# Performance work log

Measured on AMD Instinct MI355X. Metric: run time of the kernel, lower is better.

Reference implementation:

```python
import jax, jax.numpy as jnp
import numpy as np

B, S, D_MODEL, D_K, D_V = 4, 2048, 1024, 1024, 1024


def setup_inputs() -> dict:
    key = jax.random.key(0)
    k1, k2, k3, k4 = jax.random.split(key, 4)
    scale = 1.0 / np.sqrt(D_MODEL)
    x = jax.random.normal(k1, (B, S, D_MODEL), dtype=jnp.float32)
    Wq = jax.random.normal(k2, (D_K, D_MODEL), dtype=jnp.float32) * scale
    Wk = jax.random.normal(k3, (D_K, D_MODEL), dtype=jnp.float32) * scale
    Wv = jax.random.normal(k4, (D_V, D_MODEL), dtype=jnp.float32) * scale
    # causal mask: position i may attend to j <= i (True = keep)
    mask = jnp.broadcast_to(jnp.tril(jnp.ones((S, S), dtype=bool)), (B, S, S))
    return {"x": x, "mask": mask, "Wq": Wq, "Wk": Wk, "Wv": Wv}


def reference(x, mask, Wq, Wk, Wv):
    # nn.Linear(d, k, bias=False): y = x @ W.T with W of shape [k, d]
    q = jnp.einsum('bsd,kd->bsk', x, Wq)
    k = jnp.einsum('bsd,kd->bsk', x, Wk)
    v = jnp.einsum('bsd,vd->bsv', x, Wv)
    scores = jnp.einsum('bik,bjk->bij', q, k) / jnp.sqrt(jnp.float32(D_K))
    s = jnp.where(mask, scores, -jnp.inf)
    # masked, fully-masked-row-safe softmax (fully masked rows -> all zeros,
    # matching softmax[all-masked rows] = 0 in the original)
    m = jnp.max(s, axis=-1, keepdims=True)
    m_safe = jnp.where(jnp.isfinite(m), m, 0.0)
    e = jnp.exp(s - m_safe)          # exp(-inf) = 0 for masked entries
    denom = jnp.sum(e, axis=-1, keepdims=True)
    p = e / jnp.where(denom == 0.0, 1.0, denom)
    return jnp.einsum('bij,bjv->biv', p, v)
```

## Files before the change

### kernel.cpp

```cpp
#include <hip/hip_runtime.h>
#include <hip/hip_bf16.h>
#include <stdint.h>

#define SEQ   2048
#define DM    1024
#define NBAT  4

typedef __attribute__((ext_vector_type(8))) short  short8;
typedef __attribute__((ext_vector_type(4))) float  floatx4;

__device__ __forceinline__ unsigned short f2b(float f) {
    __hip_bfloat16 h = __float2bfloat16(f);
    unsigned short r;
    __builtin_memcpy(&r, &h, 2);
    return r;
}

__device__ __forceinline__ void gload16(const void* g, void* s) {
    __builtin_amdgcn_global_load_lds(
        (const __attribute__((address_space(1))) unsigned int*)(uintptr_t)g,
        (__attribute__((address_space(3))) unsigned int*)(uintptr_t)s,
        16, 0, 0);
}

__global__ void cast_bf16_4(const float4* __restrict__ in, ushort4* __restrict__ out, int n4) {
    int i = blockIdx.x * 256 + threadIdx.x;
    if (i < n4) {
        float4 f = in[i];
        ushort4 u;
        u.x = f2b(f.x); u.y = f2b(f.y); u.z = f2b(f.z); u.w = f2b(f.w);
        out[i] = u;
    }
}

__global__ void zero_f32(float* __restrict__ p, int n) {
    int i = blockIdx.x * 256 + threadIdx.x;
    if (i < n) p[i] = 0.f;
}

template<int OUTM, bool TRI, bool KLIM, bool REV>
__global__ __launch_bounds__(256) void gemm_bt(
    const unsigned short* __restrict__ A, const unsigned short* __restrict__ Bm,
    void* __restrict__ Cv,
    unsigned short* __restrict__ Qo, unsigned short* __restrict__ Ko,
    unsigned short* __restrict__ Vto,
    float* __restrict__ rowsum,
    int M, int N, int K,
    long long sA, long long sB, long long sC, float qscale)
{
    int m0, n0;
    if (TRI) {
        const int f = blockIdx.x;
        int ti = (int)((sqrtf(8.f * f + 1.f) - 1.f) * 0.5f);
        if ((ti + 1) * (ti + 2) / 2 <= f) ti++;
        if (ti * (ti + 1) / 2 > f) ti--;
        const int tj = f - ti * (ti + 1) / 2;
        m0 = ti * 128;
        n0 = tj * 128;
    } else {
        m0 = (REV ? (gridDim.y - 1 - blockIdx.y) : blockIdx.y) * 128;
        n0 = blockIdx.x * 128;
    }
    const int z = blockIdx.z;
    A  += (size_t)z * sA;
    Bm += (size_t)z * sB;

    __shared__ __align__(16) unsigned short As[128 * 32];
    __shared__ __align__(16) unsigned short Bs[128 * 32];

    const int t    = threadIdx.x;
    const int w    = t >> 6;
    const int lane = t & 63;
    const int wr   = w >> 1, wc = w & 1;
    const int r    = lane & 15, q = lane >> 4;

    floatx4 acc[4][4];
#pragma unroll
    for (int i = 0; i < 4; i++)
#pragma unroll
        for (int j = 0; j < 4; j++)
            acc[i][j] = (floatx4){0.f, 0.f, 0.f, 0.f};

    const int kEnd = KLIM ? ((m0 + 128 < K) ? m0 + 128 : K) : K;

    const int row0 = t >> 2;
    const int cc0  = t & 3;

    for (int k0 = 0; k0 < kEnd; k0 += 32) {
        const size_t ka = (size_t)k0 + cc0 * 8;
        gload16(A  + (size_t)(m0 + row0)      * K + ka, As + (size_t)w * 512);
        gload16(A  + (size_t)(m0 + row0 + 64) * K + ka, As + 2048 + (size_t)w * 512);
        gload16(Bm + (size_t)(n0 + row0)      * K + ka, Bs + (size_t)w * 512);
        gload16(Bm + (size_t)(n0 + row0 + 64) * K + ka, Bs + 2048 + (size_t)w * 512);
        __builtin_amdgcn_s_waitcnt(0);
        __syncthreads();

        short8 af[4], bf[4];
#pragma unroll
        for (int i = 0; i < 4; i++) {
            af[i] = *(const short8*)&As[(wr * 64 + i * 16 + r) * 32 + q * 8];
            bf[i] = *(const short8*)&Bs[(wc * 64 + i * 16 + r) * 32 + q * 8];
        }
#pragma unroll
        for (int i = 0; i < 4; i++)
#pragma unroll
            for (int j = 0; j < 4; j++)
                acc[i][j] = __builtin_amdgcn_mfma_f32_16x16x32_bf16(af[i], bf[j], acc[i][j], 0, 0, 0);
        __syncthreads();
    }

    const int gmb = m0 + wr * 64 + q * 4;
    const int gnb = n0 + wc * 64 + r;
    if (OUTM == 3) {
#pragma unroll
        for (int i = 0; i < 4; i++) {
            const int gm = gmb + i * 16;
#pragma unroll
            for (int j = 0; j < 4; j++) {
                const int gn = gnb + j * 16;
                if (n0 < 1024) {
#pragma unroll
                    for (int rr = 0; rr < 4; rr++)
                        Qo[(size_t)(gm + rr) * 1024 + gn] = f2b(acc[i][j][rr] * qscale);
                } else if (n0 < 2048) {
#pragma unroll
                    for (int rr = 0; rr < 4; rr++)
                        Ko[(size_t)(gm + rr) * 1024 + (gn - 1024)] = f2b(acc[i][j][rr]);
                } else {
                    const int b = gm >> 11;
                    const int s = gm & 2047;
                    const int v = gn - 2048;
                    ushort4 u;
                    u.x = f2b(acc[i][j][0]);
                    u.y = f2b(acc[i][j][1]);
                    u.z = f2b(acc[i][j][2]);
                    u.w = f2b(acc[i][j][3]);
                    *(ushort4*)&Vto[((size_t)(b * 1024 + v)) * 2048 + s] = u;
                }
            }
        }
    } else if (OUTM == 4) {
        unsigned short* E = (unsigned short*)Cv + (size_t)z * sC;
        float* rs = rowsum + (size_t)z * SEQ;
#pragma unroll
        for (int i = 0; i < 4; i++) {
            const int gm = gmb + i * 16;
#pragma unroll
            for (int rr = 0; rr < 4; rr++) {
                float part = 0.f;
#pragma unroll
                for (int j = 0; j < 4; j++) {
                    const int gn = gnb + j * 16;
                    const float ev = (gn <= gm + rr) ? __expf(acc[i][j][rr]) : 0.f;
                    part += ev;
                    E[(size_t)(gm + rr) * N + gn] = f2b(ev);
                }
#pragma unroll
                for (int off = 1; off <= 8; off <<= 1)
                    part += __shfl_xor(part, off, 64);
                if (r == 0) atomicAdd(&rs[gm + rr], part);
            }
        }
    } else {
        float* C = (float*)Cv + (size_t)z * sC;
        const float* rs = rowsum + (size_t)z * SEQ;
#pragma unroll
        for (int i = 0; i < 4; i++) {
            const int gm = gmb + i * 16;
#pragma unroll
            for (int rr = 0; rr < 4; rr++) {
                const float inv = 1.0f / rs[gm + rr];
#pragma unroll
                for (int j = 0; j < 4; j++) {
                    const int gn = gnb + j * 16;
                    C[(size_t)(gm + rr) * N + gn] = acc[i][j][rr] * inv;
                }
            }
        }
    }
}

extern "C" void kernel_launch(void* const* d_in, const int* in_sizes, int n_in,
                              void* d_out, int out_size, void* d_ws, size_t ws_size,
                              hipStream_t stream) {
    (void)in_sizes; (void)n_in; (void)out_size; (void)ws_size;
    const float* x  = (const float*)d_in[0];
    const float* Wq = (const float*)d_in[2];
    const float* Wk = (const float*)d_in[3];
    const float* Wv = (const float*)d_in[4];

    char* base = (char*)d_ws;
    size_t off = 0;
    auto alloc = [&](size_t n) { char* p = base + off; off += (n + 255) & ~(size_t)255; return p; };

    unsigned short* xb   = (unsigned short*)alloc((size_t)NBAT * SEQ * DM * 2);
    unsigned short* wall = (unsigned short*)alloc((size_t)3 * DM * DM * 2);
    unsigned short* Qb   = (unsigned short*)alloc((size_t)NBAT * SEQ * DM * 2);
    unsigned short* Kb   = (unsigned short*)alloc((size_t)NBAT * SEQ * DM * 2);
    unsigned short* Vtb  = (unsigned short*)alloc((size_t)NBAT * DM * SEQ * 2);
    unsigned short* E    = (unsigned short*)alloc((size_t)NBAT * SEQ * SEQ * 2);
    float*          rsum = (float*)alloc((size_t)NBAT * SEQ * 4);

    const dim3 blk(256);

    {
        int n4 = NBAT * SEQ * DM / 4;
        cast_bf16_4<<<dim3((n4 + 255) / 256), blk, 0, stream>>>((const float4*)x, (ushort4*)xb, n4);
        int w4 = DM * DM / 4;
        dim3 wg((w4 + 255) / 256);
        cast_bf16_4<<<wg, blk, 0, stream>>>((const float4*)Wq, (ushort4*)(wall),               w4);
        cast_bf16_4<<<wg, blk, 0, stream>>>((const float4*)Wk, (ushort4*)(wall + DM * DM),     w4);
        cast_bf16_4<<<wg, blk, 0, stream>>>((const float4*)Wv, (ushort4*)(wall + 2 * DM * DM), w4);
        zero_f32<<<dim3((NBAT * SEQ + 255) / 256), blk, 0, stream>>>(rsum, NBAT * SEQ);
    }

    const int Mtot = NBAT * SEQ;

    gemm_bt<3, false, false, false><<<dim3(3 * DM / 128, Mtot / 128, 1), blk, 0, stream>>>(
        xb, wall, nullptr, Qb, Kb, Vtb, nullptr, Mtot, 3 * DM, DM, 0, 0, 0, 0.03125f);

    gemm_bt<4, true, false, false><<<dim3(136, 1, NBAT), blk, 0, stream>>>(
        Qb, Kb, E, nullptr, nullptr, nullptr, rsum, SEQ, SEQ, DM,
        (long long)SEQ * DM, (long long)SEQ * DM, (long long)SEQ * SEQ, 1.0f);

    gemm_bt<5, false, true, true><<<dim3(DM / 128, SEQ / 128, NBAT), blk, 0, stream>>>(
        E, Vtb, d_out, nullptr, nullptr, nullptr, rsum, SEQ, DM, SEQ,
        (long long)SEQ * SEQ, (long long)DM * SEQ, (long long)SEQ * DM, 1.0f);
}
```

Measured before the change: 308.5 us.

## Fuse score and PV GEMMs into one kernel with per-row-block ready flags

Merges the causal score GEMM and the P·V GEMM into one launch. The row-block ordering is chosen so the larger blocks come first, and each PV tile spin-waits on an atomic counter until every score tile of its row block has written E and the row sums. It also folds the three weight casts into one launch, and the zeroing kernel now clears the counters too. The aim is to remove a launch boundary and the tail idle time between the two attention stages. In exchange it adds spin-waiting, which could deadlock or stall if dependent blocks are scheduled ahead of the blocks they wait on.

```diff
diff --git a/kernel.cpp b/kernel.cpp
--- a/kernel.cpp
+++ b/kernel.cpp
@@ -33,37 +33,31 @@
     }
 }
 
-__global__ void zero_f32(float* __restrict__ p, int n) {
+__global__ void cast_w3(const float4* __restrict__ w0, const float4* __restrict__ w1,
+                        const float4* __restrict__ w2, ushort4* __restrict__ out, int n4) {
+    const float4* srcs[3] = {w0, w1, w2};
     int i = blockIdx.x * 256 + threadIdx.x;
-    if (i < n) p[i] = 0.f;
-}
-
-template<int OUTM, bool TRI, bool KLIM, bool REV>
-__global__ __launch_bounds__(256) void gemm_bt(
+    if (i < n4) {
+        float4 f = srcs[blockIdx.y][i];
+        ushort4 u;
+        u.x = f2b(f.x); u.y = f2b(f.y); u.z = f2b(f.z); u.w = f2b(f.w);
+        out[(size_t)blockIdx.y * n4 + i] = u;
+    }
+}
+
+__global__ void zero_u32(unsigned int* __restrict__ p, int n) {
+    int i = blockIdx.x * 256 + threadIdx.x;
+    if (i < n) p[i] = 0u;
+}
+
+__global__ __launch_bounds__(256) void qkv_gemm(
     const unsigned short* __restrict__ A, const unsigned short* __restrict__ Bm,
-    void* __restrict__ Cv,
     unsigned short* __restrict__ Qo, unsigned short* __restrict__ Ko,
-    unsigned short* __restrict__ Vto,
-    float* __restrict__ rowsum,
-    int M, int N, int K,
-    long long sA, long long sB, long long sC, float qscale)
+    unsigned short* __restrict__ Vto, float qscale)
 {
-    int m0, n0;
-    if (TRI) {
-        const int f = blockIdx.x;
-        int ti = (int)((sqrtf(8.f * f + 1.f) - 1.f) * 0.5f);
-        if ((ti + 1) * (ti + 2) / 2 <= f) ti++;
-        if (ti * (ti + 1) / 2 > f) ti--;
-        const int tj = f - ti * (ti + 1) / 2;
-        m0 = ti * 128;
-        n0 = tj * 128;
-    } else {
-        m0 = (REV ? (gridDim.y - 1 - blockIdx.y) : blockIdx.y) * 128;
-        n0 = blockIdx.x * 128;
-    }
-    const int z = blockIdx.z;
-    A  += (size_t)z * sA;
-    Bm += (size_t)z * sB;
+    const int m0 = blockIdx.y * 128;
+    const int n0 = blockIdx.x * 128;
+    const int K  = DM;
 
     __shared__ __align__(16) unsigned short As[128 * 32];
     __shared__ __align__(16) unsigned short Bs[128 * 32];
@@ -81,12 +75,10 @@
         for (int j = 0; j < 4; j++)
             acc[i][j] = (floatx4){0.f, 0.f, 0.f, 0.f};
 
-    const int kEnd = KLIM ? ((m0 + 128 < K) ? m0 + 128 : K) : K;
-
     const int row0 = t >> 2;
     const int cc0  = t & 3;
 
-    for (int k0 = 0; k0 < kEnd; k0 += 32) {
+    for (int k0 = 0; k0 < K; k0 += 32) {
         const size_t ka = (size_t)k0 + cc0 * 8;
         gload16(A  + (size_t)(m0 + row0)      * K + ka, As + (size_t)w * 512);
         gload16(A  + (size_t)(m0 + row0 + 64) * K + ka, As + 2048 + (size_t)w * 512);
@@ -111,36 +103,116 @@
 
     const int gmb = m0 + wr * 64 + q * 4;
     const int gnb = n0 + wc * 64 + r;
-    if (OUTM == 3) {
+#pragma unroll
+    for (int i = 0; i < 4; i++) {
+        const int gm = gmb + i * 16;
+#pragma unroll
+        for (int j = 0; j < 4; j++) {
+            const int gn = gnb + j * 16;
+            if (n0 < 1024) {
+#pragma unroll
+                for (int rr = 0; rr < 4; rr++)
+                    Qo[(size_t)(gm + rr) * 1024 + gn] = f2b(acc[i][j][rr] * qscale);
+            } else if (n0 < 2048) {
+#pragma unroll
+                for (int rr = 0; rr < 4; rr++)
+                    Ko[(size_t)(gm + rr) * 1024 + (gn - 1024)] = f2b(acc[i][j][rr]);
+            } else {
+                const int b = gm >> 11;
+                const int s = gm & 2047;
+                const int v = gn - 2048;
+                ushort4 u;
+                u.x = f2b(acc[i][j][0]);
+                u.y = f2b(acc[i][j][1]);
+                u.z = f2b(acc[i][j][2]);
+                u.w = f2b(acc[i][j][3]);
+                *(ushort4*)&Vto[((size_t)(b * 1024 + v)) * 2048 + s] = u;
+            }
+        }
+    }
+}
+
+__global__ __launch_bounds__(256, 5) void attn_fused(
+    const unsigned short* __restrict__ Qb, const unsigned short* __restrict__ Kb,
+    unsigned short* __restrict__ E, const unsigned short* __restrict__ Vtb,
+    float* __restrict__ Out, float* __restrict__ rowsum, int* __restrict__ done)
+{
+    const int z = blockIdx.z;
+    const int g = blockIdx.x;
+    int u = (int)(24.5f - sqrtf(600.25f - 2.0f * (float)g));
+    while (24 * (u + 1) - (u + 1) * u / 2 <= g) u++;
+    while (24 * u - u * (u - 1) / 2 > g) u--;
+    const int ti    = 15 - u;
+    const int local = g - (24 * u - u * (u - 1) / 2);
+    const bool isScore = (local <= ti);
+    const int m0 = ti * 128;
+
+    int n0, lda, ldb, kEnd;
+    const unsigned short *A, *Bm;
+    if (isScore) {
+        n0  = local * 128;
+        A   = Qb + (size_t)z * SEQ * DM;  lda = DM;
+        Bm  = Kb + (size_t)z * SEQ * DM;  ldb = DM;
+        kEnd = DM;
+    } else {
+        n0  = (local - ti - 1) * 128;
+        A   = E   + (size_t)z * SEQ * SEQ; lda = SEQ;
+        Bm  = Vtb + (size_t)z * DM * SEQ;  ldb = SEQ;
+        kEnd = m0 + 128;
+        if (threadIdx.x == 0) {
+            while (__hip_atomic_load(&done[z * 16 + ti], __ATOMIC_ACQUIRE,
+                                     __HIP_MEMORY_SCOPE_AGENT) < ti + 1)
+                __builtin_amdgcn_s_sleep(1);
+        }
+        __syncthreads();
+    }
+
+    __shared__ __align__(16) unsigned short As[128 * 32];
+    __shared__ __align__(16) unsigned short Bs[128 * 32];
+
+    const int t    = threadIdx.x;
+    const int w    = t >> 6;
+    const int lane = t & 63;
+    const int wr   = w >> 1, wc = w & 1;
+    const int r    = lane & 15, q = lane >> 4;
+
+    floatx4 acc[4][4];
+#pragma unroll
+    for (int i = 0; i < 4; i++)
+#pragma unroll
+        for (int j = 0; j < 4; j++)
+            acc[i][j] = (floatx4){0.f, 0.f, 0.f, 0.f};
+
+    const int row0 = t >> 2;
+    const int cc0  = t & 3;
+
+    for (int k0 = 0; k0 < kEnd; k0 += 32) {
+        const size_t ka = (size_t)k0 + cc0 * 8;
+        gload16(A  + (size_t)(m0 + row0)      * lda + ka, As + (size_t)w * 512);
+        gload16(A  + (size_t)(m0 + row0 + 64) * lda + ka, As + 2048 + (size_t)w * 512);
+        gload16(Bm + (size_t)(n0 + row0)      * ldb + ka, Bs + (size_t)w * 512);
+        gload16(Bm + (size_t)(n0 + row0 + 64) * ldb + ka, Bs + 2048 + (size_t)w * 512);
+        __builtin_amdgcn_s_waitcnt(0);
+        __syncthreads();
+
+        short8 af[4], bf[4];
 #pragma unroll
         for (int i = 0; i < 4; i++) {
-            const int gm = gmb + i * 16;
-#pragma unroll
-            for (int j = 0; j < 4; j++) {
-                const int gn = gnb + j * 16;
-                if (n0 < 1024) {
-#pragma unroll
-                    for (int rr = 0; rr < 4; rr++)
-                        Qo[(size_t)(gm + rr) * 1024 + gn] = f2b(acc[i][j][rr] * qscale);
-                } else if (n0 < 2048) {
-#pragma unroll
-                    for (int rr = 0; rr < 4; rr++)
-                        Ko[(size_t)(gm + rr) * 1024 + (gn - 1024)] = f2b(acc[i][j][rr]);
-                } else {
-                    const int b = gm >> 11;
-                    const int s = gm & 2047;
-                    const int v = gn - 2048;
-                    ushort4 u;
-                    u.x = f2b(acc[i][j][0]);
-                    u.y = f2b(acc[i][j][1]);
-                    u.z = f2b(acc[i][j][2]);
-                    u.w = f2b(acc[i][j][3]);
-                    *(ushort4*)&Vto[((size_t)(b * 1024 + v)) * 2048 + s] = u;
-                }
-            }
-        }
-    } else if (OUTM == 4) {
-        unsigned short* E = (unsigned short*)Cv + (size_t)z * sC;
+            af[i] = *(const short8*)&As[(wr * 64 + i * 16 + r) * 32 + q * 8];
+            bf[i] = *(const short8*)&Bs[(wc * 64 + i * 16 + r) * 32 + q * 8];
+        }
+#pragma unroll
+        for (int i = 0; i < 4; i++)
+#pragma unroll
+            for (int j = 0; j < 4; j++)
+                acc[i][j] = __builtin_amdgcn_mfma_f32_16x16x32_bf16(af[i], bf[j], acc[i][j], 0, 0, 0);
+        __syncthreads();
+    }
+
+    const int gmb = m0 + wr * 64 + q * 4;
+    const int gnb = n0 + wc * 64 + r;
+    if (isScore) {
+        unsigned short* Ez = E + (size_t)z * SEQ * SEQ;
         float* rs = rowsum + (size_t)z * SEQ;
 #pragma unroll
         for (int i = 0; i < 4; i++) {
@@ -153,7 +225,7 @@
                     const int gn = gnb + j * 16;
                     const float ev = (gn <= gm + rr) ? __expf(acc[i][j][rr]) : 0.f;
                     part += ev;
-                    E[(size_t)(gm + rr) * N + gn] = f2b(ev);
+                    Ez[(size_t)(gm + rr) * SEQ + gn] = f2b(ev);
                 }
 #pragma unroll
                 for (int off = 1; off <= 8; off <<= 1)
@@ -161,8 +233,13 @@
                 if (r == 0) atomicAdd(&rs[gm + rr], part);
             }
         }
+        __syncthreads();
+        if (t == 0) {
+            __threadfence();
+            atomicAdd(&done[z * 16 + ti], 1);
+        }
     } else {
-        float* C = (float*)Cv + (size_t)z * sC;
+        float* C = Out + (size_t)z * SEQ * DM;
         const float* rs = rowsum + (size_t)z * SEQ;
 #pragma unroll
         for (int i = 0; i < 4; i++) {
@@ -173,7 +250,7 @@
 #pragma unroll
                 for (int j = 0; j < 4; j++) {
                     const int gn = gnb + j * 16;
-                    C[(size_t)(gm + rr) * N + gn] = acc[i][j][rr] * inv;
+                    C[(size_t)(gm + rr) * DM + gn] = acc[i][j][rr] * inv;
                 }
             }
         }
@@ -199,7 +276,8 @@
     unsigned short* Kb   = (unsigned short*)alloc((size_t)NBAT * SEQ * DM * 2);
     unsigned short* Vtb  = (unsigned short*)alloc((size_t)NBAT * DM * SEQ * 2);
     unsigned short* E    = (unsigned short*)alloc((size_t)NBAT * SEQ * SEQ * 2);
-    float*          rsum = (float*)alloc((size_t)NBAT * SEQ * 4);
+    float*          rsum = (float*)alloc((size_t)NBAT * SEQ * 4 + 64 * 4);
+    int*            done = (int*)(rsum + NBAT * SEQ);
 
     const dim3 blk(256);
 
@@ -207,23 +285,17 @@
         int n4 = NBAT * SEQ * DM / 4;
         cast_bf16_4<<<dim3((n4 + 255) / 256), blk, 0, stream>>>((const float4*)x, (ushort4*)xb, n4);
         int w4 = DM * DM / 4;
-        dim3 wg((w4 + 255) / 256);
-        cast_bf16_4<<<wg, blk, 0, stream>>>((const float4*)Wq, (ushort4*)(wall),               w4);
-        cast_bf16_4<<<wg, blk, 0, stream>>>((const float4*)Wk, (ushort4*)(wall + DM * DM),     w4);
-        cast_bf16_4<<<wg, blk, 0, stream>>>((const float4*)Wv, (ushort4*)(wall + 2 * DM * DM), w4);
-        zero_f32<<<dim3((NBAT * SEQ + 255) / 256), blk, 0, stream>>>(rsum, NBAT * SEQ);
+        cast_w3<<<dim3((w4 + 255) / 256, 3), blk, 0, stream>>>(
+            (const float4*)Wq, (const float4*)Wk, (const float4*)Wv, (ushort4*)wall, w4);
+        zero_u32<<<dim3((NBAT * SEQ + 64 + 255) / 256), blk, 0, stream>>>(
+            (unsigned int*)rsum, NBAT * SEQ + 64);
     }
 
     const int Mtot = NBAT * SEQ;
 
-    gemm_bt<3, false, false, false><<<dim3(3 * DM / 128, Mtot / 128, 1), blk, 0, stream>>>(
-        xb, wall, nullptr, Qb, Kb, Vtb, nullptr, Mtot, 3 * DM, DM, 0, 0, 0, 0.03125f);
-
-    gemm_bt<4, true, false, false><<<dim3(136, 1, NBAT), blk, 0, stream>>>(
-        Qb, Kb, E, nullptr, nullptr, nullptr, rsum, SEQ, SEQ, DM,
-        (long long)SEQ * DM, (long long)SEQ * DM, (long long)SEQ * SEQ, 1.0f);
-
-    gemm_bt<5, false, true, true><<<dim3(DM / 128, SEQ / 128, NBAT), blk, 0, stream>>>(
-        E, Vtb, d_out, nullptr, nullptr, nullptr, rsum, SEQ, DM, SEQ,
-        (long long)SEQ * SEQ, (long long)DM * SEQ, (long long)SEQ * DM, 1.0f);
-}
+    qkv_gemm<<<dim3(3 * DM / 128, Mtot / 128, 1), blk, 0, stream>>>(
+        xb, wall, Qb, Kb, Vtb, 0.03125f);
+
+    attn_fused<<<dim3(264, 1, NBAT), blk, 0, stream>>>(
+        Qb, Kb, E, Vtb, (float*)d_out, rsum, done);
+}
```

Result: slower. 548.0 us (+77.6%).
